# Performance work log

Hardware: AMD Instinct MI355X
Metric: run time of the kernel (lower is better)

Reference implementation:

```python
import jax, jax.numpy as jnp
import numpy as np


def setup_inputs() -> dict:
    key = jax.random.key(0)
    k1, k2, k3 = jax.random.split(key, 3)
    B, C, H, W = 4, 32, 256, 256
    nw, nh = 16, 16
    K = nw * nh
    pixel_feats = jax.random.normal(k1, (B, C, H, W), dtype=jnp.float32)
    assoc_map = jax.random.uniform(k2, (B, 9, H, W), dtype=jnp.float32)
    index_map = jax.random.randint(k3, (B, H, W), 0, K, dtype=jnp.int32)
    return {
        "pixel_feats": pixel_feats,
        "assoc_map": assoc_map,
        "index_map": index_map,
        "nw_spixels": nw,
        "nh_spixels": nh,
    }


def reference(pixel_feats, assoc_map, index_map, nw_spixels, nh_spixels):
    # pixel_feats: [B,C,H,W], assoc_map: [B,9,H,W] (3x3 superpixel-neighbor
    # association weights, row-major (dy,dx) in {-1,0,1}^2), index_map: [B,H,W]
    # base superpixel id in [0, nw*nh). Output: [B, C, nw*nh].
    B, C, H, W = pixel_feats.shape
    K = nw_spixels * nh_spixels
    P = H * W

    idx = index_map.reshape(B, P).astype(jnp.int32)
    ix = idx % nw_spixels  # base spixel grid x
    iy = idx // nw_spixels  # base spixel grid y

    # 9 relative offsets over the superpixel grid
    dy, dx = jnp.meshgrid(jnp.arange(-1, 2), jnp.arange(-1, 2), indexing="ij")
    dy = dy.reshape(9)
    dx = dx.reshape(9)

    tx = ix[:, None, :] + dx[None, :, None]  # [B,9,P]
    ty = iy[:, None, :] + dy[None, :, None]
    valid = (tx >= 0) & (tx < nw_spixels) & (ty >= 0) & (ty < nh_spixels)
    tgt = jnp.where(valid, ty * nw_spixels + tx, 0)  # [B,9,P]

    w = assoc_map.reshape(B, 9, P) * valid.astype(assoc_map.dtype)  # [B,9,P]

    # fold batch into segment id so a single segment_sum handles all images
    seg = (tgt + jnp.arange(B, dtype=jnp.int32)[:, None, None] * K).reshape(-1)

    wsum = jax.ops.segment_sum(w.reshape(-1), seg, num_segments=B * K)  # [B*K]

    # weighted pixel features scattered into superpixel bins
    contrib = w[:, :, None, :] * pixel_feats.reshape(B, 1, C, P)  # [B,9,C,P]
    contrib = contrib.transpose(0, 1, 3, 2).reshape(-1, C)  # [B*9*P, C]
    fsum = jax.ops.segment_sum(contrib, seg, num_segments=B * K)  # [B*K, C]

    eps = 1e-16
    denom = jnp.where(wsum > eps, wsum, 1.0)
    sp = jnp.where(wsum[:, None] > eps, fsum / denom[:, None], 0.0)
    return sp.reshape(B, K, C).transpose(0, 2, 1)  # [B,C,K]
```

## Files before the change

kernel.cpp:

```cpp
#include <hip/hip_runtime.h>
#include <hip/hip_bf16.h>


#define CCH  32
#define TPB  1024
#define PPB  1024
#define GTPB 512
#define CAPC 384
#define RECW 24
#define CNTS 16
#define KMAX 256

__device__ __forceinline__ unsigned pack_bf16(float a, float b) {
    unsigned ua = __float_as_uint(a);
    unsigned ub = __float_as_uint(b);
    ua = (ua + 0x7FFFu + ((ua >> 16) & 1u)) >> 16;
    ub = (ub + 0x7FFFu + ((ub >> 16) & 1u)) >> 16;
    return ua | (ub << 16);
}

__global__ __launch_bounds__(TPB) void spx_prep_kernel(
    const float* __restrict__ pf,
    const float* __restrict__ assoc,
    const int*   __restrict__ idxmap,
    const int*   __restrict__ nw_p,
    const int*   __restrict__ nh_p,
    int*         __restrict__ cnt,
    unsigned*    __restrict__ recs,
    float*       __restrict__ ovf,
    int P, int K, int cap, int bpb)
{
    __shared__ int hist[KMAX];
    __shared__ int bases[KMAX];

    const int b   = blockIdx.x / bpb;
    const int blk = blockIdx.x - b * bpb;
    const int tid = threadIdx.x;
    const int p   = blk * PPB + tid;

    if (tid < KMAX) hist[tid] = 0;
    __syncthreads();

    const int*   ix_b = idxmap + (size_t)b * P;
    const float* pf_b = pf     + (size_t)b * CCH * P;
    const float* as_b = assoc  + (size_t)b * 9 * P;

    const int idx  = ix_b[p];
    const int rank = atomicAdd(&hist[idx], 1);

    unsigned u[16];
#pragma unroll
    for (int c2 = 0; c2 < 16; ++c2) {
        const float f0 = pf_b[(size_t)(2*c2  ) * P + p];
        const float f1 = pf_b[(size_t)(2*c2+1) * P + p];
        u[c2] = pack_bf16(f0, f1);
    }
    float wv[9];
#pragma unroll
    for (int j = 0; j < 9; ++j) wv[j] = as_b[(size_t)j * P + p];

    __syncthreads();
    if (tid < KMAX)
        bases[tid] = atomicAdd(&cnt[(b * K + tid) * CNTS], hist[tid]);
    __syncthreads();

    const int pos = bases[idx] + rank;

    if (pos < cap) {
        unsigned* dst = recs + ((size_t)(b * K + idx) * cap + pos) * RECW;
        uint4* d4 = (uint4*)dst;
        d4[0] = make_uint4(u[0],  u[1],  u[2],  u[3]);
        d4[1] = make_uint4(u[4],  u[5],  u[6],  u[7]);
        d4[2] = make_uint4(u[8],  u[9],  u[10], u[11]);
        d4[3] = make_uint4(u[12], u[13], u[14], u[15]);
        d4[4] = make_uint4(pack_bf16(wv[0], wv[1]), pack_bf16(wv[2], wv[3]),
                           pack_bf16(wv[4], wv[5]), pack_bf16(wv[6], wv[7]));
        dst[20] = pack_bf16(wv[8], 0.0f);
    } else {
        const int nw = nw_p[0], nh = nh_p[0];
        const int iy = idx / nw, ixx = idx - (idx / nw) * nw;
#pragma unroll
        for (int j = 0; j < 9; ++j) {
            const int ty = iy + j / 3 - 1, tx = ixx + j % 3 - 1;
            if (tx >= 0 && tx < nw && ty >= 0 && ty < nh) {
                float* o = ovf + (size_t)(b * K + ty * nw + tx) * (CCH + 1);
#pragma unroll
                for (int c2 = 0; c2 < 16; ++c2) {
                    const float f0 = __uint_as_float(u[c2] << 16);
                    const float f1 = __uint_as_float(u[c2] & 0xFFFF0000u);
                    unsafeAtomicAdd(&o[2*c2],     wv[j] * f0);
                    unsafeAtomicAdd(&o[2*c2 + 1], wv[j] * f1);
                }
                unsafeAtomicAdd(&o[CCH], wv[j]);
            }
        }
    }
}

__global__ __launch_bounds__(GTPB) void spx_gather_kernel(
    const unsigned* __restrict__ recs,
    const int*      __restrict__ cnt,
    const float*    __restrict__ ovf,
    const int*      __restrict__ nw_p,
    const int*      __restrict__ nh_p,
    float*          __restrict__ out,
    int P, int K, int cap)
{
    __shared__ int   jcnt[9], jsrc[9];
    __shared__ float red[128][CCH + 1];
    __shared__ float red2[8][CCH + 1];

    const int b   = blockIdx.x / K;
    const int k   = blockIdx.x - b * K;
    const int tid = threadIdx.x;
    const int nw  = nw_p[0];
    const int nh  = nh_p[0];
    const int ky  = k / nw;
    const int kx  = k - ky * nw;

    if (tid < 9) {
        const int dy = tid / 3 - 1, dx = tid % 3 - 1;
        const int sy = ky - dy, sx = kx - dx;
        const bool v = (sx >= 0) & (sx < nw) & (sy >= 0) & (sy < nh);
        const int src = v ? (b * K + sy * nw + sx) : 0;
        int c = v ? cnt[src * CNTS] : 0;
        if (c > cap) c = cap;
        jcnt[tid] = c;
        jsrc[tid] = src;
    }
    __syncthreads();

    const int l = tid & 3;
    const int g = tid >> 2;

    float a[8] = {0.f, 0.f, 0.f, 0.f, 0.f, 0.f, 0.f, 0.f};
    float wacc = 0.f;

#pragma unroll
    for (int j = 0; j < 9; ++j) {
        const int c = jcnt[j];
        const unsigned* rb = recs + (size_t)jsrc[j] * cap * RECW;
        for (int i = g; i < c; i += 128) {
            const unsigned* r = rb + (size_t)i * RECW;
            const uint4 u = *(const uint4*)(r + 4 * l);
            const unsigned wp = r[16 + (j >> 1)];
            const float w = (j & 1) ? __uint_as_float(wp & 0xFFFF0000u)
                                    : __uint_as_float(wp << 16);
            a[0] += w * __uint_as_float(u.x << 16);
            a[1] += w * __uint_as_float(u.x & 0xFFFF0000u);
            a[2] += w * __uint_as_float(u.y << 16);
            a[3] += w * __uint_as_float(u.y & 0xFFFF0000u);
            a[4] += w * __uint_as_float(u.z << 16);
            a[5] += w * __uint_as_float(u.z & 0xFFFF0000u);
            a[6] += w * __uint_as_float(u.w << 16);
            a[7] += w * __uint_as_float(u.w & 0xFFFF0000u);
            wacc += w;
        }
    }

#pragma unroll
    for (int t = 0; t < 8; ++t) red[g][8 * l + t] = a[t];
    if (l == 0) red[g][CCH] = wacc;
    __syncthreads();

    if (tid < 264) {
        const int col = tid >> 3, part = tid & 7;
        float s = 0.f;
#pragma unroll
        for (int r2 = 0; r2 < 16; ++r2) s += red[part * 16 + r2][col];
        red2[part][col] = s;
    }
    __syncthreads();

    if (tid < CCH + 1) {
        float s = 0.f;
#pragma unroll
        for (int r2 = 0; r2 < 8; ++r2) s += red2[r2][tid];
        s += ovf[(size_t)(b * K + k) * (CCH + 1) + tid];
        red2[0][tid] = s;
    }
    __syncthreads();

    if (tid < CCH) {
        const float W = red2[0][CCH];
        out[((size_t)b * CCH + tid) * K + k] =
            (W > 1e-16f) ? (red2[0][tid] / W) : 0.f;
    }
}

extern "C" void kernel_launch(void* const* d_in, const int* in_sizes, int n_in,
                              void* d_out, int out_size, void* d_ws, size_t ws_size,
                              hipStream_t stream) {
    const float* pf     = (const float*)d_in[0];
    const float* assoc  = (const float*)d_in[1];
    const int*   idxmap = (const int*)d_in[2];
    const int*   nw_p   = (const int*)d_in[3];
    const int*   nh_p   = (const int*)d_in[4];
    float* out = (float*)d_out;

    const int BP = in_sizes[2];
    const int B  = 4;
    const int P  = BP / B;
    const int K  = out_size / (B * CCH);

    const size_t cnt_bytes = (size_t)B * K * CNTS * sizeof(int);
    const size_t ovf_bytes = (size_t)B * K * (CCH + 1) * sizeof(float);
    int*      cnt  = (int*)d_ws;
    float*    ovf  = (float*)((char*)d_ws + cnt_bytes);
    unsigned* recs = (unsigned*)((char*)d_ws + cnt_bytes + ovf_bytes);

    size_t avail = (ws_size > cnt_bytes + ovf_bytes)
                       ? (ws_size - cnt_bytes - ovf_bytes) : 0;
    int cap = (int)(avail / ((size_t)B * K * RECW * sizeof(unsigned)));
    if (cap > CAPC) cap = CAPC;
    if (cap < 1) cap = 1;

    hipMemsetAsync(cnt, 0, cnt_bytes + ovf_bytes, stream);

    const int bpb = P / PPB;
    spx_prep_kernel<<<B * bpb, TPB, 0, stream>>>(
        pf, assoc, idxmap, nw_p, nh_p, cnt, recs, ovf, P, K, cap, bpb);

    spx_gather_kernel<<<B * K, GTPB, 0, stream>>>(
        recs, cnt, ovf, nw_p, nh_p, out, P, K, cap);
}
```

Baseline: 128.5 us.

## Split gather into per-source scan with 9-way partials and neighbor finalize

Replaces the per-target gather, which read each source bucket's records nine times (once per neighboring target), with a scan kernel that reads each bucket once and accumulates all nine weighted partial sums. A small finalize kernel then sums the nine relevant partials per target superpixel plus the overflow buffer and normalizes. This reduces redundant record traffic. In exchange it adds a partial-sum buffer in the workspace, which shrinks the available record capacity, and one extra kernel launch. Weight sums are computed in a separate serial pass by one lane per group, and the unused wa accumulator is left in place.

Result: faster. 112.4 us (-12.5%).

```diff
diff --git a/kernel.cpp b/kernel.cpp
--- a/kernel.cpp
+++ b/kernel.cpp
@@ -5,7 +5,7 @@
 #define CCH  32
 #define TPB  1024
 #define PPB  1024
-#define GTPB 512
+#define STPB 512
 #define CAPC 384
 #define RECW 24
 #define CNTS 16
@@ -17,6 +17,12 @@
     ua = (ua + 0x7FFFu + ((ua >> 16) & 1u)) >> 16;
     ub = (ub + 0x7FFFu + ((ub >> 16) & 1u)) >> 16;
     return ua | (ub << 16);
+}
+__device__ __forceinline__ float bf_lo(unsigned u) {
+    return __uint_as_float(u << 16);
+}
+__device__ __forceinline__ float bf_hi(unsigned u) {
+    return __uint_as_float(u & 0xFFFF0000u);
 }
 
 __global__ __launch_bounds__(TPB) void spx_prep_kernel(
@@ -86,10 +92,8 @@
                 float* o = ovf + (size_t)(b * K + ty * nw + tx) * (CCH + 1);
 #pragma unroll
                 for (int c2 = 0; c2 < 16; ++c2) {
-                    const float f0 = __uint_as_float(u[c2] << 16);
-                    const float f1 = __uint_as_float(u[c2] & 0xFFFF0000u);
-                    unsafeAtomicAdd(&o[2*c2],     wv[j] * f0);
-                    unsafeAtomicAdd(&o[2*c2 + 1], wv[j] * f1);
+                    unsafeAtomicAdd(&o[2*c2],     wv[j] * bf_lo(u[c2]));
+                    unsafeAtomicAdd(&o[2*c2 + 1], wv[j] * bf_hi(u[c2]));
                 }
                 unsafeAtomicAdd(&o[CCH], wv[j]);
             }
@@ -97,18 +101,94 @@
     }
 }
 
-__global__ __launch_bounds__(GTPB) void spx_gather_kernel(
+__global__ __launch_bounds__(STPB) void spx_scan_kernel(
     const unsigned* __restrict__ recs,
     const int*      __restrict__ cnt,
-    const float*    __restrict__ ovf,
-    const int*      __restrict__ nw_p,
-    const int*      __restrict__ nh_p,
-    float*          __restrict__ out,
-    int P, int K, int cap)
+    float*          __restrict__ partial,
+    int K, int cap)
 {
-    __shared__ int   jcnt[9], jsrc[9];
-    __shared__ float red[128][CCH + 1];
-    __shared__ float red2[8][CCH + 1];
+    __shared__ float red[32][9][CCH + 1];
+
+    const int bs  = blockIdx.x;
+    const int tid = threadIdx.x;
+    const int c2  = tid & 15;
+    const int g   = tid >> 4;
+
+    int c = cnt[bs * CNTS];
+    if (c > cap) c = cap;
+    const unsigned* rb = recs + (size_t)bs * cap * RECW;
+
+    float a[9][2];
+    float wa = 0.f;
+#pragma unroll
+    for (int j = 0; j < 9; ++j) { a[j][0] = 0.f; a[j][1] = 0.f; }
+
+    for (int i = g; i < c; i += 32) {
+        const unsigned* r = rb + (size_t)i * RECW;
+        const unsigned uf  = r[c2];
+        const float f0 = bf_lo(uf), f1 = bf_hi(uf);
+        const unsigned wp0 = r[16], wp1 = r[17], wp2 = r[18],
+                       wp3 = r[19], wp4 = r[20];
+        const float w[9] = { bf_lo(wp0), bf_hi(wp0), bf_lo(wp1), bf_hi(wp1),
+                             bf_lo(wp2), bf_hi(wp2), bf_lo(wp3), bf_hi(wp3),
+                             bf_lo(wp4) };
+#pragma unroll
+        for (int j = 0; j < 9; ++j) {
+            a[j][0] += w[j] * f0;
+            a[j][1] += w[j] * f1;
+        }
+        wa += w[0] + w[1] + w[2] + w[3] + w[4] + w[5] + w[6] + w[7] + w[8];
+    }
+
+    (void)wa;
+
+    float ws[9];
+#pragma unroll
+    for (int j = 0; j < 9; ++j) ws[j] = 0.f;
+    if (c2 == 0) {
+        for (int i = g; i < c; i += 32) {
+            const unsigned* r = rb + (size_t)i * RECW;
+            const unsigned wp0 = r[16], wp1 = r[17], wp2 = r[18],
+                           wp3 = r[19], wp4 = r[20];
+            ws[0] += bf_lo(wp0); ws[1] += bf_hi(wp0);
+            ws[2] += bf_lo(wp1); ws[3] += bf_hi(wp1);
+            ws[4] += bf_lo(wp2); ws[5] += bf_hi(wp2);
+            ws[6] += bf_lo(wp3); ws[7] += bf_hi(wp3);
+            ws[8] += bf_lo(wp4);
+        }
+    }
+
+#pragma unroll
+    for (int j = 0; j < 9; ++j) {
+        red[g][j][2 * c2]     = a[j][0];
+        red[g][j][2 * c2 + 1] = a[j][1];
+    }
+    if (c2 == 0) {
+#pragma unroll
+        for (int j = 0; j < 9; ++j) red[g][j][CCH] = ws[j];
+    }
+    __syncthreads();
+
+    float* pout = partial + (size_t)bs * 9 * (CCH + 1);
+    for (int col = tid; col < 9 * (CCH + 1); col += STPB) {
+        const int j  = col / (CCH + 1);
+        const int cc = col - j * (CCH + 1);
+        float s = 0.f;
+#pragma unroll
+        for (int g2 = 0; g2 < 32; ++g2) s += red[g2][j][cc];
+        pout[col] = s;
+    }
+}
+
+__global__ __launch_bounds__(64) void spx_finalize_kernel(
+    const float* __restrict__ partial,
+    const float* __restrict__ ovf,
+    const int*   __restrict__ nw_p,
+    const int*   __restrict__ nh_p,
+    float*       __restrict__ out,
+    int K)
+{
+    __shared__ float F[CCH + 1];
 
     const int b   = blockIdx.x / K;
     const int k   = blockIdx.x - b * K;
@@ -118,73 +198,25 @@
     const int ky  = k / nw;
     const int kx  = k - ky * nw;
 
-    if (tid < 9) {
-        const int dy = tid / 3 - 1, dx = tid % 3 - 1;
-        const int sy = ky - dy, sx = kx - dx;
-        const bool v = (sx >= 0) & (sx < nw) & (sy >= 0) & (sy < nh);
-        const int src = v ? (b * K + sy * nw + sx) : 0;
-        int c = v ? cnt[src * CNTS] : 0;
-        if (c > cap) c = cap;
-        jcnt[tid] = c;
-        jsrc[tid] = src;
-    }
-    __syncthreads();
-
-    const int l = tid & 3;
-    const int g = tid >> 2;
-
-    float a[8] = {0.f, 0.f, 0.f, 0.f, 0.f, 0.f, 0.f, 0.f};
-    float wacc = 0.f;
-
-#pragma unroll
-    for (int j = 0; j < 9; ++j) {
-        const int c = jcnt[j];
-        const unsigned* rb = recs + (size_t)jsrc[j] * cap * RECW;
-        for (int i = g; i < c; i += 128) {
-            const unsigned* r = rb + (size_t)i * RECW;
-            const uint4 u = *(const uint4*)(r + 4 * l);
-            const unsigned wp = r[16 + (j >> 1)];
-            const float w = (j & 1) ? __uint_as_float(wp & 0xFFFF0000u)
-                                    : __uint_as_float(wp << 16);
-            a[0] += w * __uint_as_float(u.x << 16);
-            a[1] += w * __uint_as_float(u.x & 0xFFFF0000u);
-            a[2] += w * __uint_as_float(u.y << 16);
-            a[3] += w * __uint_as_float(u.y & 0xFFFF0000u);
-            a[4] += w * __uint_as_float(u.z << 16);
-            a[5] += w * __uint_as_float(u.z & 0xFFFF0000u);
-            a[6] += w * __uint_as_float(u.w << 16);
-            a[7] += w * __uint_as_float(u.w & 0xFFFF0000u);
-            wacc += w;
-        }
-    }
-
-#pragma unroll
-    for (int t = 0; t < 8; ++t) red[g][8 * l + t] = a[t];
-    if (l == 0) red[g][CCH] = wacc;
-    __syncthreads();
-
-    if (tid < 264) {
-        const int col = tid >> 3, part = tid & 7;
-        float s = 0.f;
-#pragma unroll
-        for (int r2 = 0; r2 < 16; ++r2) s += red[part * 16 + r2][col];
-        red2[part][col] = s;
-    }
-    __syncthreads();
-
     if (tid < CCH + 1) {
-        float s = 0.f;
-#pragma unroll
-        for (int r2 = 0; r2 < 8; ++r2) s += red2[r2][tid];
-        s += ovf[(size_t)(b * K + k) * (CCH + 1) + tid];
-        red2[0][tid] = s;
+        float s = ovf[(size_t)(b * K + k) * (CCH + 1) + tid];
+#pragma unroll
+        for (int j = 0; j < 9; ++j) {
+            const int dy = j / 3 - 1, dx = j % 3 - 1;
+            const int sy = ky - dy, sx = kx - dx;
+            if (sx >= 0 && sx < nw && sy >= 0 && sy < nh) {
+                s += partial[((size_t)(b * K + sy * nw + sx) * 9 + j)
+                             * (CCH + 1) + tid];
+            }
+        }
+        F[tid] = s;
     }
     __syncthreads();
 
     if (tid < CCH) {
-        const float W = red2[0][CCH];
+        const float W = F[CCH];
         out[((size_t)b * CCH + tid) * K + k] =
-            (W > 1e-16f) ? (red2[0][tid] / W) : 0.f;
+            (W > 1e-16f) ? (F[tid] / W) : 0.f;
     }
 }
 
@@ -203,14 +235,17 @@
     const int P  = BP / B;
     const int K  = out_size / (B * CCH);
 
-    const size_t cnt_bytes = (size_t)B * K * CNTS * sizeof(int);
-    const size_t ovf_bytes = (size_t)B * K * (CCH + 1) * sizeof(float);
-    int*      cnt  = (int*)d_ws;
-    float*    ovf  = (float*)((char*)d_ws + cnt_bytes);
-    unsigned* recs = (unsigned*)((char*)d_ws + cnt_bytes + ovf_bytes);
-
-    size_t avail = (ws_size > cnt_bytes + ovf_bytes)
-                       ? (ws_size - cnt_bytes - ovf_bytes) : 0;
+    const size_t cnt_bytes  = (size_t)B * K * CNTS * sizeof(int);
+    const size_t ovf_bytes  = (size_t)B * K * (CCH + 1) * sizeof(float);
+    const size_t part_bytes = (size_t)B * K * 9 * (CCH + 1) * sizeof(float);
+    int*      cnt     = (int*)d_ws;
+    float*    ovf     = (float*)((char*)d_ws + cnt_bytes);
+    float*    partial = (float*)((char*)d_ws + cnt_bytes + ovf_bytes);
+    unsigned* recs    = (unsigned*)((char*)d_ws + cnt_bytes + ovf_bytes
+                                    + part_bytes);
+
+    size_t used = cnt_bytes + ovf_bytes + part_bytes;
+    size_t avail = (ws_size > used) ? (ws_size - used) : 0;
     int cap = (int)(avail / ((size_t)B * K * RECW * sizeof(unsigned)));
     if (cap > CAPC) cap = CAPC;
     if (cap < 1) cap = 1;
@@ -221,6 +256,8 @@
     spx_prep_kernel<<<B * bpb, TPB, 0, stream>>>(
         pf, assoc, idxmap, nw_p, nh_p, cnt, recs, ovf, P, K, cap, bpb);
 
-    spx_gather_kernel<<<B * K, GTPB, 0, stream>>>(
-        recs, cnt, ovf, nw_p, nh_p, out, P, K, cap);
-}
+    spx_scan_kernel<<<B * K, STPB, 0, stream>>>(recs, cnt, partial, K, cap);
+
+    spx_finalize_kernel<<<B * K, 64, 0, stream>>>(
+        partial, ovf, nw_p, nh_p, out, K);
+}
```
